# Performance work log

Hardware: AMD Instinct MI355X
Metric: run time of the kernel (lower is better)

The kernel has to match this reference:

```python
import jax, jax.numpy as jnp
import numpy as np

B = 131072
# join branch layer dims: 203 -> 175 -> 150 -> 128 -> 80 -> 48
DIMS = [203, 175, 150, 128, 80, 48]

def setup_inputs() -> dict:
    key = jax.random.key(0)
    ks = jax.random.split(key, 11)
    inp = {"x": jax.random.normal(ks[0], (B, DIMS[0]), dtype=jnp.float32)}
    for i in range(5):
        fan_in, fan_out = DIMS[i], DIMS[i + 1]
        bound = 1.0 / np.sqrt(fan_in)
        inp[f"W{i+1}"] = jax.random.uniform(ks[1 + 2 * i], (fan_out, fan_in), minval=-bound, maxval=bound, dtype=jnp.float32)
        inp[f"b{i+1}"] = jax.random.uniform(ks[2 + 2 * i], (fan_out,), minval=-bound, maxval=bound, dtype=jnp.float32)
    return inp

def reference(x, W1, b1, W2, b2, W3, b3, W4, b4, W5, b5):
    # join branch of NodeEmbedding, dropout in eval mode (identity).
    h = jnp.tanh(x @ W1.T + b1)      # [B,175]
    h = jnp.tanh(h @ W2.T + b2)      # [B,150]
    h = jnp.tanh(h @ W3.T + b3)      # [B,128]
    h = jnp.tanh(h @ W4.T + b4)      # [B,80]
    return h @ W5.T + b5             # [B,48], no activation on last layer
```

## Files before the change

### kernel.cpp

```cpp
#include <hip/hip_runtime.h>


typedef short short8 __attribute__((ext_vector_type(8)));
typedef float f32x16 __attribute__((ext_vector_type(16)));
typedef unsigned int uint;
typedef unsigned short ushort;

#define PSTR 116
#define PSTRU (PSTR*2)
#define NTHREADS 768
#define MROWS 64

__device__ __forceinline__ ushort f2bf(float f) {
    uint u = __float_as_uint(f);
    u += 0x7FFFu + ((u >> 16) & 1u);
    return (ushort)(u >> 16);
}
__device__ __forceinline__ float bf2f(ushort h) { return __uint_as_float(((uint)h) << 16); }
__device__ __forceinline__ float fast_tanh(float x) {
    float e = __expf(2.0f * x);
    float t = __builtin_amdgcn_rcpf(e + 1.0f);
    return fmaf(-2.0f, t, 1.0f);
}
__device__ __forceinline__ uint cvt_pk_bf16(float s0, float s1) {
    uint r;
    asm("v_cvt_pk_bf16_f32 %0, %1, %2" : "=v"(r) : "v"(s0), "v"(s1));
    return r;
}

union U4S8 { uint4 u; short8 s; };

__global__ void prep_weights(const float* __restrict__ W1, const float* __restrict__ W2,
                             const float* __restrict__ W3, const float* __restrict__ W4,
                             const float* __restrict__ W5, char* __restrict__ ws)
{
    const int b = blockIdx.x, l = threadIdx.x;
    int layer, local;
    if      (b <  78) { layer = 0; local = b; }
    else if (b < 133) { layer = 1; local = b - 78; }
    else if (b < 173) { layer = 2; local = b - 133; }
    else if (b < 197) { layer = 3; local = b - 173; }
    else              { layer = 4; local = b - 197; }
    const int NTa[5]  = {6, 5, 4, 3, 2};
    const int FINa[5] = {203, 175, 150, 128, 80};
    const int FOa[5]  = {175, 150, 128, 80, 48};
    const float* Wp = (layer == 0) ? W1 : (layer == 1) ? W2 : (layer == 2) ? W3
                    : (layer == 3) ? W4 : W5;
    const int nt = NTa[layer], fin = FINa[layer], fout = FOa[layer];
    const int c = local / nt, t = local % nt;
    const int n  = t * 32 + (l & 31);
    const int kb = c * 16 + (l >> 5) * 8;
    uint hw[4], lw[4];
#pragma unroll
    for (int j = 0; j < 8; ++j) {
        int k = kb + j;
        float v = (n < fout && k < fin) ? Wp[(size_t)n * fin + k] : 0.0f;
        ushort hh = f2bf(v);
        ushort ll = f2bf(v - bf2f(hh));
        if (j & 1) { hw[j >> 1] |= ((uint)hh) << 16; lw[j >> 1] |= ((uint)ll) << 16; }
        else       { hw[j >> 1]  = hh;               lw[j >> 1]  = ll; }
    }
    char* dst = ws + (size_t)b * 2048 + l * 16;
    *(uint4*)dst          = make_uint4(hw[0], hw[1], hw[2], hw[3]);
    *(uint4*)(dst + 1024) = make_uint4(lw[0], lw[1], lw[2], lw[3]);
}

template<int KC, int NT, int FOUT, int PADN, bool ACT, bool LAST>
__device__ __forceinline__ void run_layer(const char* __restrict__ wsL,
    const float* __restrict__ bias, uint* aH, uint* aL, float* outg,
    int row0, int l, int rg, int t, int lx, int lh, int tid)
{
    f32x16 acc;
    {
        float bv = 0.0f;
        if (t < NT) { int n = t * 32 + lx; bv = (n < FOUT) ? bias[n] : 0.0f; }
#pragma unroll
        for (int r = 0; r < 16; ++r) acc[r] = bv;
    }

    if (t < NT) {
        const char* ha = (const char*)aH + (rg * 32 + lx) * (PSTR * 4) + lh * 16;
        const char* la = (const char*)aL + (rg * 32 + lx) * (PSTR * 4) + lh * 16;
        const uint4* wsb = (const uint4*)wsL + (size_t)(t * 2) * 64 + l;

        U4S8 bhA, blA, ahA, alA, bhB, blB, ahB, alB;
        bhA.u = wsb[0];
        blA.u = wsb[64];
        ahA.u = *(const uint4*)(ha);
        alA.u = *(const uint4*)(la);

#pragma unroll
        for (int c = 0; c < KC; ++c) {
            const bool ev = ((c & 1) == 0);
            U4S8& bh = ev ? bhA : bhB;  U4S8& bl = ev ? blA : blB;
            U4S8& ah = ev ? ahA : ahB;  U4S8& al = ev ? alA : alB;
            if (c + 1 < KC) {
                U4S8& nbh = ev ? bhB : bhA;  U4S8& nbl = ev ? blB : blA;
                U4S8& nah = ev ? ahB : ahA;  U4S8& nal = ev ? alB : alA;
                const uint4* wpn = wsb + (size_t)((c + 1) * NT * 2) * 64;
                nbh.u = wpn[0];
                nbl.u = wpn[64];
                nah.u = *(const uint4*)(ha + (c + 1) * 32);
                nal.u = *(const uint4*)(la + (c + 1) * 32);
            }
            acc = __builtin_amdgcn_mfma_f32_32x32x16_bf16(ah.s, bh.s, acc, 0, 0, 0);
            acc = __builtin_amdgcn_mfma_f32_32x32x16_bf16(al.s, bh.s, acc, 0, 0, 0);
            acc = __builtin_amdgcn_mfma_f32_32x32x16_bf16(ah.s, bl.s, acc, 0, 0, 0);
        }
    }
    if (!LAST) __syncthreads();

    if (t < NT) {
        ushort* pH = (ushort*)aH;
        ushort* pL = (ushort*)aL;
        const int col = t * 32 + lx;
        const int rbase = rg * 32;
#pragma unroll
        for (int i = 0; i < 8; ++i) {
            float v0 = acc[2 * i], v1 = acc[2 * i + 1];
            if (ACT) { v0 = fast_tanh(v0); v1 = fast_tanh(v1); }
            const int r0 = 2 * i;
            const int rowl = rbase + (r0 & 3) + 8 * (r0 >> 2) + 4 * lh;
            if (LAST) {
                if (col < 48) {
                    outg[(size_t)(row0 + rowl) * 48 + col]     = v0;
                    outg[(size_t)(row0 + rowl + 1) * 48 + col] = v1;
                }
            } else if (col < FOUT) {
                uint chi = cvt_pk_bf16(v0, v1);
                float h0 = __uint_as_float(chi << 16);
                float h1 = __uint_as_float(chi & 0xFFFF0000u);
                uint clo = cvt_pk_bf16(v0 - h0, v1 - h1);
                pH[rowl * PSTRU + col]       = (ushort)chi;
                pH[(rowl + 1) * PSTRU + col] = (ushort)(chi >> 16);
                pL[rowl * PSTRU + col]       = (ushort)clo;
                pL[(rowl + 1) * PSTRU + col] = (ushort)(clo >> 16);
            }
        }
    }
    if (!LAST) {
        if (PADN > 0) {
            ushort* pH = (ushort*)aH;
            ushort* pL = (ushort*)aL;
            for (int idx = tid; idx < MROWS * PADN; idx += NTHREADS) {
                int row = idx / PADN, p = idx % PADN;
                pH[row * PSTRU + FOUT + p] = 0;
                pL[row * PSTRU + FOUT + p] = 0;
            }
        }
        __syncthreads();
    }
}

__global__ __launch_bounds__(NTHREADS, 4)
void mlp_mfma(const float* __restrict__ x,
              const float* __restrict__ b1, const float* __restrict__ b2,
              const float* __restrict__ b3, const float* __restrict__ b4,
              const float* __restrict__ b5,
              const char* __restrict__ ws, float* __restrict__ out)
{
    __shared__ __align__(16) uint aH[MROWS * PSTR];
    __shared__ __align__(16) uint aL[MROWS * PSTR];

    const int tid = threadIdx.x;
    const int l = tid & 63, w = tid >> 6;
    const int rg = w / 6, t = w - 6 * rg;
    const int lx = l & 31, lh = l >> 5;
    const int row0 = blockIdx.x * MROWS;

    for (int e = tid; e < MROWS * 104; e += NTHREADS) {
        int row = e / 104, dcol = e - row * 104;
        int col = dcol * 2;
        const float* xp = x + (size_t)(row0 + row) * 203;
        float v0 = (col < 203) ? xp[col] : 0.0f;
        float v1 = (col + 1 < 203) ? xp[col + 1] : 0.0f;
        uint chi = cvt_pk_bf16(v0, v1);
        float h0 = __uint_as_float(chi << 16);
        float h1 = __uint_as_float(chi & 0xFFFF0000u);
        uint clo = cvt_pk_bf16(v0 - h0, v1 - h1);
        aH[row * PSTR + dcol] = chi;
        aL[row * PSTR + dcol] = clo;
    }
    __syncthreads();

    run_layer<13, 6, 175,  1, true,  false>(ws,              b1, aH, aL, nullptr, row0, l, rg, t, lx, lh, tid);
    run_layer<11, 5, 150, 10, true,  false>(ws +  78 * 2048, b2, aH, aL, nullptr, row0, l, rg, t, lx, lh, tid);
    run_layer<10, 4, 128,  0, true,  false>(ws + 133 * 2048, b3, aH, aL, nullptr, row0, l, rg, t, lx, lh, tid);
    run_layer< 8, 3,  80,  0, true,  false>(ws + 173 * 2048, b4, aH, aL, nullptr, row0, l, rg, t, lx, lh, tid);
    run_layer< 5, 2,  48,  0, false, true >(ws + 197 * 2048, b5, aH, aL, out,     row0, l, rg, t, lx, lh, tid);
}

extern "C" void kernel_launch(void* const* d_in, const int* in_sizes, int n_in,
                              void* d_out, int out_size, void* d_ws, size_t ws_size,
                              hipStream_t stream) {
    (void)in_sizes; (void)n_in; (void)ws_size; (void)out_size;
    const float* x  = (const float*)d_in[0];
    const float* W1 = (const float*)d_in[1];
    const float* b1 = (const float*)d_in[2];
    const float* W2 = (const float*)d_in[3];
    const float* b2 = (const float*)d_in[4];
    const float* W3 = (const float*)d_in[5];
    const float* b3 = (const float*)d_in[6];
    const float* W4 = (const float*)d_in[7];
    const float* b4 = (const float*)d_in[8];
    const float* W5 = (const float*)d_in[9];
    const float* b5 = (const float*)d_in[10];
    float* out = (float*)d_out;
    char* ws = (char*)d_ws;

    hipLaunchKernelGGL(prep_weights, dim3(207), dim3(64), 0, stream,
                       W1, W2, W3, W4, W5, ws);
    hipLaunchKernelGGL(mlp_mfma, dim3(131072 / MROWS), dim3(NTHREADS), 0, stream,
                       x, b1, b2, b3, b4, b5, ws, out);
}
```

Baseline: 279.1 us.

## Swap MFMA operand order for row-major accumulators, vectorize epilogue, pad biases

Swaps the MFMA A/B operands so each lane's accumulator holds four consecutive output features of one row. That allows packed uint2 LDS stores of the bf16 hi/lo activations and float4 global stores for the output, replacing scattered 16-bit and scalar writes. Biases are copied into a zero-padded workspace table by an extra prep block, which removes the per-layer padding-zero loop and the bias bounds checks. Weight loads now prefetch two chunks ahead using a triple buffer with a sched_barrier, at the cost of more registers.

After: 280.7 us. No clear change (+0.6%).

```diff
diff --git a/kernel.cpp b/kernel.cpp
--- a/kernel.cpp
+++ b/kernel.cpp
@@ -7,9 +7,9 @@
 typedef unsigned short ushort;
 
 #define PSTR 116
-#define PSTRU (PSTR*2)
 #define NTHREADS 768
 #define MROWS 64
+#define BIAS_OFF (207 * 2048)
 
 __device__ __forceinline__ ushort f2bf(float f) {
     uint u = __float_as_uint(f);
@@ -32,9 +32,22 @@
 
 __global__ void prep_weights(const float* __restrict__ W1, const float* __restrict__ W2,
                              const float* __restrict__ W3, const float* __restrict__ W4,
-                             const float* __restrict__ W5, char* __restrict__ ws)
+                             const float* __restrict__ W5,
+                             const float* __restrict__ b1, const float* __restrict__ b2,
+                             const float* __restrict__ b3, const float* __restrict__ b4,
+                             const float* __restrict__ b5, char* __restrict__ ws)
 {
     const int b = blockIdx.x, l = threadIdx.x;
+    const int FOa[5]  = {175, 150, 128, 80, 48};
+    if (b == 207) {
+        float* bp = (float*)(ws + BIAS_OFF);
+        const float* bs[5] = {b1, b2, b3, b4, b5};
+        for (int i = l; i < 5 * 192; i += 64) {
+            int L = i / 192, j = i - L * 192;
+            bp[i] = (j < FOa[L]) ? bs[L][j] : 0.0f;
+        }
+        return;
+    }
     int layer, local;
     if      (b <  78) { layer = 0; local = b; }
     else if (b < 133) { layer = 1; local = b - 78; }
@@ -43,7 +56,6 @@
     else              { layer = 4; local = b - 197; }
     const int NTa[5]  = {6, 5, 4, 3, 2};
     const int FINa[5] = {203, 175, 150, 128, 80};
-    const int FOa[5]  = {175, 150, 128, 80, 48};
     const float* Wp = (layer == 0) ? W1 : (layer == 1) ? W2 : (layer == 2) ? W3
                     : (layer == 3) ? W4 : W5;
     const int nt = NTa[layer], fin = FINa[layer], fout = FOa[layer];
@@ -65,98 +77,88 @@
     *(uint4*)(dst + 1024) = make_uint4(lw[0], lw[1], lw[2], lw[3]);
 }
 
-template<int KC, int NT, int FOUT, int PADN, bool ACT, bool LAST>
+template<int KC, int NT, int FOUT, bool ACT, bool LAST>
 __device__ __forceinline__ void run_layer(const char* __restrict__ wsL,
-    const float* __restrict__ bias, uint* aH, uint* aL, float* outg,
-    int row0, int l, int rg, int t, int lx, int lh, int tid)
+    const float* __restrict__ biasP, uint* aH, uint* aL, float* outg,
+    int row0, int l, int rg, int t, int lx, int lh)
 {
     f32x16 acc;
-    {
-        float bv = 0.0f;
-        if (t < NT) { int n = t * 32 + lx; bv = (n < FOUT) ? bias[n] : 0.0f; }
-#pragma unroll
-        for (int r = 0; r < 16; ++r) acc[r] = bv;
-    }
-
     if (t < NT) {
+        const float4* bp = (const float4*)(biasP + t * 32 + 4 * lh);
+#pragma unroll
+        for (int q = 0; q < 4; ++q) {
+            float4 bv = bp[q * 2];
+            acc[4 * q + 0] = bv.x; acc[4 * q + 1] = bv.y;
+            acc[4 * q + 2] = bv.z; acc[4 * q + 3] = bv.w;
+        }
+
         const char* ha = (const char*)aH + (rg * 32 + lx) * (PSTR * 4) + lh * 16;
         const char* la = (const char*)aL + (rg * 32 + lx) * (PSTR * 4) + lh * 16;
         const uint4* wsb = (const uint4*)wsL + (size_t)(t * 2) * 64 + l;
 
-        U4S8 bhA, blA, ahA, alA, bhB, blB, ahB, alB;
-        bhA.u = wsb[0];
-        blA.u = wsb[64];
-        ahA.u = *(const uint4*)(ha);
-        alA.u = *(const uint4*)(la);
+        U4S8 wh[3], wl[3], ah[2], al[2];
+        wh[0].u = wsb[0];                  wl[0].u = wsb[64];
+        wh[1].u = wsb[(size_t)NT * 128];   wl[1].u = wsb[(size_t)NT * 128 + 64];
+        ah[0].u = *(const uint4*)ha;       al[0].u = *(const uint4*)la;
 
 #pragma unroll
         for (int c = 0; c < KC; ++c) {
-            const bool ev = ((c & 1) == 0);
-            U4S8& bh = ev ? bhA : bhB;  U4S8& bl = ev ? blA : blB;
-            U4S8& ah = ev ? ahA : ahB;  U4S8& al = ev ? alA : alB;
+            if (c + 2 < KC) {
+                wh[(c + 2) % 3].u = wsb[(size_t)(c + 2) * NT * 128];
+                wl[(c + 2) % 3].u = wsb[(size_t)(c + 2) * NT * 128 + 64];
+            }
             if (c + 1 < KC) {
-                U4S8& nbh = ev ? bhB : bhA;  U4S8& nbl = ev ? blB : blA;
-                U4S8& nah = ev ? ahB : ahA;  U4S8& nal = ev ? alB : alA;
-                const uint4* wpn = wsb + (size_t)((c + 1) * NT * 2) * 64;
-                nbh.u = wpn[0];
-                nbl.u = wpn[64];
-                nah.u = *(const uint4*)(ha + (c + 1) * 32);
-                nal.u = *(const uint4*)(la + (c + 1) * 32);
-            }
-            acc = __builtin_amdgcn_mfma_f32_32x32x16_bf16(ah.s, bh.s, acc, 0, 0, 0);
-            acc = __builtin_amdgcn_mfma_f32_32x32x16_bf16(al.s, bh.s, acc, 0, 0, 0);
-            acc = __builtin_amdgcn_mfma_f32_32x32x16_bf16(ah.s, bl.s, acc, 0, 0, 0);
+                ah[(c + 1) & 1].u = *(const uint4*)(ha + (c + 1) * 32);
+                al[(c + 1) & 1].u = *(const uint4*)(la + (c + 1) * 32);
+            }
+            __builtin_amdgcn_sched_barrier(0);
+            acc = __builtin_amdgcn_mfma_f32_32x32x16_bf16(wh[c % 3].s, ah[c & 1].s, acc, 0, 0, 0);
+            acc = __builtin_amdgcn_mfma_f32_32x32x16_bf16(wh[c % 3].s, al[c & 1].s, acc, 0, 0, 0);
+            acc = __builtin_amdgcn_mfma_f32_32x32x16_bf16(wl[c % 3].s, ah[c & 1].s, acc, 0, 0, 0);
         }
     }
     if (!LAST) __syncthreads();
 
     if (t < NT) {
-        ushort* pH = (ushort*)aH;
-        ushort* pL = (ushort*)aL;
-        const int col = t * 32 + lx;
-        const int rbase = rg * 32;
-#pragma unroll
-        for (int i = 0; i < 8; ++i) {
-            float v0 = acc[2 * i], v1 = acc[2 * i + 1];
-            if (ACT) { v0 = fast_tanh(v0); v1 = fast_tanh(v1); }
-            const int r0 = 2 * i;
-            const int rowl = rbase + (r0 & 3) + 8 * (r0 >> 2) + 4 * lh;
-            if (LAST) {
-                if (col < 48) {
-                    outg[(size_t)(row0 + rowl) * 48 + col]     = v0;
-                    outg[(size_t)(row0 + rowl + 1) * 48 + col] = v1;
+        const int rowb = rg * 32 + lx;
+        if (LAST) {
+#pragma unroll
+            for (int q = 0; q < 4; ++q) {
+                const int f = t * 32 + 8 * q + 4 * lh;
+                if (f + 3 < 48) {
+                    float4 v = make_float4(acc[4 * q], acc[4 * q + 1],
+                                           acc[4 * q + 2], acc[4 * q + 3]);
+                    *(float4*)(outg + (size_t)(row0 + rowb) * 48 + f) = v;
                 }
-            } else if (col < FOUT) {
-                uint chi = cvt_pk_bf16(v0, v1);
-                float h0 = __uint_as_float(chi << 16);
-                float h1 = __uint_as_float(chi & 0xFFFF0000u);
-                uint clo = cvt_pk_bf16(v0 - h0, v1 - h1);
-                pH[rowl * PSTRU + col]       = (ushort)chi;
-                pH[(rowl + 1) * PSTRU + col] = (ushort)(chi >> 16);
-                pL[rowl * PSTRU + col]       = (ushort)clo;
-                pL[(rowl + 1) * PSTRU + col] = (ushort)(clo >> 16);
-            }
-        }
-    }
-    if (!LAST) {
-        if (PADN > 0) {
-            ushort* pH = (ushort*)aH;
-            ushort* pL = (ushort*)aL;
-            for (int idx = tid; idx < MROWS * PADN; idx += NTHREADS) {
-                int row = idx / PADN, p = idx % PADN;
-                pH[row * PSTRU + FOUT + p] = 0;
-                pL[row * PSTRU + FOUT + p] = 0;
-            }
-        }
-        __syncthreads();
-    }
+            }
+        } else {
+            uint* pHd = aH + rowb * PSTR;
+            uint* pLd = aL + rowb * PSTR;
+#pragma unroll
+            for (int q = 0; q < 4; ++q) {
+                float t0 = acc[4 * q], t1 = acc[4 * q + 1];
+                float t2 = acc[4 * q + 2], t3 = acc[4 * q + 3];
+                if (ACT) { t0 = fast_tanh(t0); t1 = fast_tanh(t1);
+                           t2 = fast_tanh(t2); t3 = fast_tanh(t3); }
+                uint h01 = cvt_pk_bf16(t0, t1);
+                uint h23 = cvt_pk_bf16(t2, t3);
+                float r0 = t0 - __uint_as_float(h01 << 16);
+                float r1 = t1 - __uint_as_float(h01 & 0xFFFF0000u);
+                float r2 = t2 - __uint_as_float(h23 << 16);
+                float r3 = t3 - __uint_as_float(h23 & 0xFFFF0000u);
+                uint l01 = cvt_pk_bf16(r0, r1);
+                uint l23 = cvt_pk_bf16(r2, r3);
+                const int dcol = t * 16 + 4 * q + 2 * lh;
+                *(uint2*)(pHd + dcol) = make_uint2(h01, h23);
+                *(uint2*)(pLd + dcol) = make_uint2(l01, l23);
+            }
+        }
+    }
+    if (!LAST) __syncthreads();
 }
 
 __global__ __launch_bounds__(NTHREADS, 4)
 void mlp_mfma(const float* __restrict__ x,
-              const float* __restrict__ b1, const float* __restrict__ b2,
-              const float* __restrict__ b3, const float* __restrict__ b4,
-              const float* __restrict__ b5,
               const char* __restrict__ ws, float* __restrict__ out)
 {
     __shared__ __align__(16) uint aH[MROWS * PSTR];
@@ -167,6 +169,7 @@
     const int rg = w / 6, t = w - 6 * rg;
     const int lx = l & 31, lh = l >> 5;
     const int row0 = blockIdx.x * MROWS;
+    const float* biasT = (const float*)(ws + BIAS_OFF);
 
     for (int e = tid; e < MROWS * 104; e += NTHREADS) {
         int row = e / 104, dcol = e - row * 104;
@@ -183,11 +186,11 @@
     }
     __syncthreads();
 
-    run_layer<13, 6, 175,  1, true,  false>(ws,              b1, aH, aL, nullptr, row0, l, rg, t, lx, lh, tid);
-    run_layer<11, 5, 150, 10, true,  false>(ws +  78 * 2048, b2, aH, aL, nullptr, row0, l, rg, t, lx, lh, tid);
-    run_layer<10, 4, 128,  0, true,  false>(ws + 133 * 2048, b3, aH, aL, nullptr, row0, l, rg, t, lx, lh, tid);
-    run_layer< 8, 3,  80,  0, true,  false>(ws + 173 * 2048, b4, aH, aL, nullptr, row0, l, rg, t, lx, lh, tid);
-    run_layer< 5, 2,  48,  0, false, true >(ws + 197 * 2048, b5, aH, aL, out,     row0, l, rg, t, lx, lh, tid);
+    run_layer<13, 6, 175, true,  false>(ws,              biasT,       aH, aL, nullptr, row0, l, rg, t, lx, lh);
+    run_layer<11, 5, 150, true,  false>(ws +  78 * 2048, biasT + 192, aH, aL, nullptr, row0, l, rg, t, lx, lh);
+    run_layer<10, 4, 128, true,  false>(ws + 133 * 2048, biasT + 384, aH, aL, nullptr, row0, l, rg, t, lx, lh);
+    run_layer< 8, 3,  80, true,  false>(ws + 173 * 2048, biasT + 576, aH, aL, nullptr, row0, l, rg, t, lx, lh);
+    run_layer< 5, 2,  48, false, true >(ws + 197 * 2048, biasT + 768, aH, aL, out,     row0, l, rg, t, lx, lh);
 }
 
 extern "C" void kernel_launch(void* const* d_in, const int* in_sizes, int n_in,
@@ -208,8 +211,8 @@
     float* out = (float*)d_out;
     char* ws = (char*)d_ws;
 
-    hipLaunchKernelGGL(prep_weights, dim3(207), dim3(64), 0, stream,
-                       W1, W2, W3, W4, W5, ws);
+    hipLaunchKernelGGL(prep_weights, dim3(208), dim3(64), 0, stream,
+                       W1, W2, W3, W4, W5, b1, b2, b3, b4, b5, ws);
     hipLaunchKernelGGL(mlp_mfma, dim3(131072 / MROWS), dim3(NTHREADS), 0, stream,
-                       x, b1, b2, b3, b4, b5, ws, out);
-}
+                       x, ws, out);
+}
```
